# Kernel optimization log

Measured on AMD Instinct MI355X. Metric: run time of the kernel, lower is better.

## Reference

```python
import jax, jax.numpy as jnp
import numpy as np

HEADS = 16
HEAD_DIM = 128


def rotate_half(x):
    x1, x2 = x[..., : x.shape[-1] // 2], x[..., x.shape[-1] // 2 :]
    return jnp.concatenate((-x2, x1), axis=-1)


def setup_inputs() -> dict:
    key = jax.random.key(0)
    ks = jax.random.split(key, 8)
    b, s, h = 2, 2048, 2048
    d = HEAD_DIM
    sc = 1.0 / np.sqrt(h)
    x = jax.random.normal(ks[0], (b, s, h), jnp.float32)
    # real RoPE angles for realism
    inv_freq = 1.0 / (10000.0 ** (jnp.arange(0, d, 2, dtype=jnp.float32) / d))
    t = jnp.arange(s, dtype=jnp.float32)
    freqs = jnp.outer(t, inv_freq)  # [s, d/2]
    emb = jnp.concatenate((freqs, freqs), axis=-1)  # [s, d]
    return {
        "x": x,
        "cos": jnp.cos(emb),
        "sin": jnp.sin(emb),
        "wq": jax.random.normal(ks[1], (h, h), jnp.float32) * sc,
        "bq": jnp.zeros((h,), jnp.float32),
        "wk": jax.random.normal(ks[2], (h, h), jnp.float32) * sc,
        "bk": jnp.zeros((h,), jnp.float32),
        "wv": jax.random.normal(ks[3], (h, h), jnp.float32) * sc,
        "bv": jnp.zeros((h,), jnp.float32),
        "wo": jax.random.normal(ks[4], (h, h), jnp.float32) * sc,
    }


def reference(x, cos, sin, wq, bq, wk, bk, wv, bv, wo):
    b, s, hidden = x.shape
    nh, d = HEADS, HEAD_DIM
    # QKV projections (F.linear: x @ W.T + b)
    def split_heads(t):
        return t.reshape(b, s, nh, d).transpose(0, 2, 1, 3)  # [b,h,s,d]
    q = split_heads(x @ wq.T + bq)
    k = split_heads(x @ wk.T + bk)
    v = split_heads(x @ wv.T + bv)
    # RoPE (cos/sin: [s,d] broadcast over [b,h,s,d])
    q = q * cos + rotate_half(q) * sin
    k = k * cos + rotate_half(k) * sin
    # full (non-causal) attention, materializing [b,h,s,s] scores as original
    scale = 1.0 / jnp.sqrt(jnp.asarray(d, x.dtype))
    scores = jnp.einsum("bhqd,bhkd->bhqk", q, k) * scale
    attn = jax.nn.softmax(scores, axis=-1)
    out = jnp.einsum("bhqk,bhkd->bhqd", attn, v)  # [b,h,s,d]
    out = out.transpose(0, 2, 1, 3).reshape(b, s, hidden)
    # o_proj: no bias
    return out @ wo.T
```

## Files before the change

### kernel.cpp

```cpp
#include <hip/hip_runtime.h>

#define B_  2
#define NH  16
#define S_  2048
#define D_  128
#define HID 2048

typedef _Float16 half_t;
typedef _Float16 f16x8 __attribute__((ext_vector_type(8)));
typedef _Float16 f16x4_t __attribute__((ext_vector_type(4)));
typedef float f32x4 __attribute__((ext_vector_type(4)));

__device__ __forceinline__ void glds16(const half_t* g, half_t* l) {
    __builtin_amdgcn_global_load_lds(
        (const __attribute__((address_space(1))) void*)g,
        (__attribute__((address_space(3))) void*)l, 16, 0, 0);
}
__device__ __forceinline__ float fexp2(float x) { return __builtin_amdgcn_exp2f(x); }

__global__ __launch_bounds__(256) void cvt_all(
    const float* __restrict__ x,  const float* __restrict__ wq, const float* __restrict__ wk,
    const float* __restrict__ wv, const float* __restrict__ wo, half_t* __restrict__ dst)
{
    long i = ((long)blockIdx.x * 256 + threadIdx.x) * 4;
    const float* src; long off;
    if (i < 8388608)       { src = x;  off = i; }
    else if (i < 12582912) { src = wq; off = i - 8388608; }
    else if (i < 16777216) { src = wk; off = i - 12582912; }
    else if (i < 20971520) { src = wv; off = i - 16777216; }
    else                   { src = wo; off = i - 20971520; }
    float4 v = *(const float4*)(src + off);
    f16x4_t h;
    h[0] = (half_t)v.x; h[1] = (half_t)v.y; h[2] = (half_t)v.z; h[3] = (half_t)v.w;
    *(f16x4_t*)(dst + i) = h;
}

__global__ __launch_bounds__(256, 3) void qkv_gemm(
    const half_t* __restrict__ xb,
    const half_t* __restrict__ wqb, const half_t* __restrict__ wkb, const half_t* __restrict__ wvb,
    const float* __restrict__ bq, const float* __restrict__ bk, const float* __restrict__ bv,
    const float* __restrict__ cosp, const float* __restrict__ sinp,
    half_t* __restrict__ qo, half_t* __restrict__ ko, half_t* __restrict__ vto)
{
    __shared__ __align__(16) half_t As[128 * 32];
    __shared__ __align__(16) half_t Bs[128 * 32];
    const int m0 = blockIdx.x * 128;
    const int n0 = blockIdx.y * 128;
    const int z  = blockIdx.z;
    const half_t* wb   = (z == 0) ? wqb : (z == 1) ? wkb : wvb;
    const float*  bias = (z == 0) ? bq  : (z == 1) ? bk  : bv;
    const int tid = threadIdx.x, wave = tid >> 6, lane = tid & 63;
    const int quad = lane >> 4, lrow = lane & 15;
    const int wm = wave >> 1, wn = wave & 1;

    const int r0 = wave * 32 + (lane >> 2);
    const int r1 = r0 + 16;
    const int c0 = (((lane & 3) - (r0 >> 1)) & 3) * 8;
    const int c1 = (((lane & 3) - (r1 >> 1)) & 3) * 8;
    const half_t* ag0 = xb + (size_t)(m0 + r0) * HID + c0;
    const half_t* ag1 = xb + (size_t)(m0 + r1) * HID + c1;
    const half_t* bg0 = wb + (size_t)(n0 + r0) * HID + c0;
    const half_t* bg1 = wb + (size_t)(n0 + r1) * HID + c1;
    half_t* al0 = &As[(wave * 32) * 32];
    half_t* al1 = &As[(wave * 32 + 16) * 32];
    half_t* bl0 = &Bs[(wave * 32) * 32];
    half_t* bl1 = &Bs[(wave * 32 + 16) * 32];

    f32x4 acc[4][4] = {};

    for (int k0 = 0; k0 < HID; k0 += 32) {
        __syncthreads();
        glds16(ag0 + k0, al0);
        glds16(ag1 + k0, al1);
        glds16(bg0 + k0, bl0);
        glds16(bg1 + k0, bl1);
        __syncthreads();
        f16x8 af[4], bf[4];
#pragma unroll
        for (int mt = 0; mt < 4; mt++) {
            const int ra = wm * 64 + mt * 16 + lrow;
            const int pa = (quad + (ra >> 1)) & 3;
            af[mt] = *(const f16x8*)&As[ra * 32 + pa * 8];
        }
#pragma unroll
        for (int nt = 0; nt < 4; nt++) {
            const int rb = wn * 16 + nt * 32 + lrow;
            const int pb = (quad + (rb >> 1)) & 3;
            bf[nt] = *(const f16x8*)&Bs[rb * 32 + pb * 8];
        }
#pragma unroll
        for (int mt = 0; mt < 4; mt++)
#pragma unroll
            for (int nt = 0; nt < 4; nt++)
                acc[mt][nt] = __builtin_amdgcn_mfma_f32_16x16x32_f16(af[mt], bf[nt], acc[mt][nt], 0, 0, 0);
    }

    const int head = blockIdx.y;
    float bs_[4];
#pragma unroll
    for (int nt = 0; nt < 4; nt++) bs_[nt] = bias[n0 + nt * 32 + wn * 16 + lrow];
#pragma unroll
    for (int mt = 0; mt < 4; mt++) {
#pragma unroll
        for (int r = 0; r < 4; r++) {
            const int m  = m0 + wm * 64 + mt * 16 + quad * 4 + r;
            const int bb = m >> 11;
            const int st = m & (S_ - 1);
            float res[4];
#pragma unroll
            for (int nt = 0; nt < 4; nt++) res[nt] = acc[mt][nt][r] + bs_[nt];
            if (z < 2) {
                const float* cr = cosp + st * D_;
                const float* sr = sinp + st * D_;
#pragma unroll
                for (int pr = 0; pr < 2; pr++) {
                    const int dlo = pr * 32 + wn * 16 + lrow;
                    float cl = cr[dlo], sl = sr[dlo], ch = cr[dlo + 64], sh = sr[dlo + 64];
                    float lo = res[pr], hi = res[pr + 2];
                    res[pr]     = lo * cl - hi * sl;
                    res[pr + 2] = hi * ch + lo * sh;
                }
                half_t* dst = (z == 0 ? qo : ko) + ((size_t)(bb * NH + head) * S_ + st) * D_;
#pragma unroll
                for (int nt = 0; nt < 4; nt++) dst[nt * 32 + wn * 16 + lrow] = (half_t)res[nt];
            } else {
                half_t* dst = vto + (size_t)(bb * NH + head) * D_ * S_ + st;
#pragma unroll
                for (int nt = 0; nt < 4; nt++) dst[(size_t)(nt * 32 + wn * 16 + lrow) * S_] = (half_t)res[nt];
            }
        }
    }
}

#define PLD 72
__global__ __launch_bounds__(256, 2) void attn_kernel(
    const half_t* __restrict__ qb, const half_t* __restrict__ kb,
    const half_t* __restrict__ vtb, half_t* __restrict__ ob)
{
    __shared__ __align__(16) half_t ks[64 * 128];
    __shared__ __align__(16) half_t vs[128 * 64];
    __shared__ __align__(16) half_t ps[4 * 32 * PLD];
    const int head = blockIdx.y, b = blockIdx.z;
    const int bh = b * NH + head;
    const int tid = threadIdx.x, wave = tid >> 6, lane = tid & 63;
    const int quad = lane >> 4, lrow = lane & 15;
    const float SC = 0.08838834764831845f * 1.4426950408889634f;
    const int q0 = blockIdx.x * 128 + wave * 32;

    f16x8 qf[2][4];
#pragma unroll
    for (int mt = 0; mt < 2; mt++) {
        const half_t* qrow = qb + ((size_t)bh * S_ + q0 + mt * 16 + lrow) * D_;
#pragma unroll
        for (int kc = 0; kc < 4; kc++) {
            f16x8 v = *(const f16x8*)(qrow + kc * 32 + quad * 8);
#pragma unroll
            for (int j = 0; j < 8; j++) v[j] = (half_t)((float)v[j] * SC);
            qf[mt][kc] = v;
        }
    }

    const half_t* kbase = kb + (size_t)bh * S_ * D_;
    const half_t* vbase = vtb + (size_t)bh * D_ * S_;
    const int pbase = wave * 32 * PLD;

    float m_run[2] = {-1e30f, -1e30f}, l_run[2] = {0.f, 0.f};
    f32x4 o[2][8] = {};

    for (int kt = 0; kt < 32; kt++) {
        __syncthreads();
#pragma unroll
        for (int i = 0; i < 4; i++) {
            const int rk = wave * 16 + i * 4 + (lane >> 4);
            const int ck = (((lane & 15) - (rk & 7)) & 15) * 8;
            glds16(kbase + (size_t)(kt * 64 + rk) * D_ + ck, &ks[(wave * 16 + i * 4) * 128]);
            const int rv = wave * 32 + i * 8 + (lane >> 3);
            const int cv = (((lane & 7) - (rv & 7)) & 7) * 8;
            glds16(vbase + (size_t)rv * S_ + kt * 64 + cv, &vs[(wave * 32 + i * 8) * 64]);
        }
        __syncthreads();

        f32x4 st[2][4] = {};
#pragma unroll
        for (int nt = 0; nt < 4; nt++) {
            const int rk2 = nt * 16 + lrow;
#pragma unroll
            for (int kc = 0; kc < 4; kc++) {
                const int pk = (kc * 4 + quad + (rk2 & 7)) & 15;
                f16x8 kf = *(const f16x8*)&ks[rk2 * 128 + pk * 8];
                st[0][nt] = __builtin_amdgcn_mfma_f32_16x16x32_f16(kf, qf[0][kc], st[0][nt], 0, 0, 0);
                st[1][nt] = __builtin_amdgcn_mfma_f32_16x16x32_f16(kf, qf[1][kc], st[1][nt], 0, 0, 0);
            }
        }

        bool upd = false;
        float alpha[2];
#pragma unroll
        for (int mt = 0; mt < 2; mt++) {
            float m01 = fmaxf(fmaxf(st[mt][0][0], st[mt][0][1]), fmaxf(st[mt][0][2], st[mt][0][3]));
            float m11 = fmaxf(fmaxf(st[mt][1][0], st[mt][1][1]), fmaxf(st[mt][1][2], st[mt][1][3]));
            float m21 = fmaxf(fmaxf(st[mt][2][0], st[mt][2][1]), fmaxf(st[mt][2][2], st[mt][2][3]));
            float m31 = fmaxf(fmaxf(st[mt][3][0], st[mt][3][1]), fmaxf(st[mt][3][2], st[mt][3][3]));
            float mx = fmaxf(fmaxf(m01, m11), fmaxf(m21, m31));
            mx = fmaxf(mx, __shfl_xor(mx, 16));
            mx = fmaxf(mx, __shfl_xor(mx, 32));
            const float mnew = fmaxf(m_run[mt], mx);
            alpha[mt] = fexp2(m_run[mt] - mnew);
            upd = upd || (mnew > m_run[mt]);
            m_run[mt] = mnew;
            float rs = 0.f;
#pragma unroll
            for (int nt = 0; nt < 4; nt++) {
                f16x4_t pk4;
#pragma unroll
                for (int r = 0; r < 4; r++) {
                    float p = fexp2(st[mt][nt][r] - mnew);
                    rs += p;
                    pk4[r] = (half_t)p;
                }
                *(f16x4_t*)&ps[pbase + (mt * 16 + lrow) * PLD + nt * 16 + quad * 4] = pk4;
            }
            rs += __shfl_xor(rs, 16);
            rs += __shfl_xor(rs, 32);
            l_run[mt] = l_run[mt] * alpha[mt] + rs;
        }
        if (__any(upd)) {
#pragma unroll
            for (int mt = 0; mt < 2; mt++) {
                float ab[4];
#pragma unroll
                for (int r = 0; r < 4; r++) ab[r] = __shfl(alpha[mt], quad * 4 + r, 16);
#pragma unroll
                for (int dt = 0; dt < 8; dt++)
#pragma unroll
                    for (int r = 0; r < 4; r++) o[mt][dt][r] *= ab[r];
            }
        }

#pragma unroll
        for (int kc2 = 0; kc2 < 2; kc2++) {
            f16x8 pf0 = *(const f16x8*)&ps[pbase + lrow * PLD + kc2 * 32 + quad * 8];
            f16x8 pf1 = *(const f16x8*)&ps[pbase + (16 + lrow) * PLD + kc2 * 32 + quad * 8];
#pragma unroll
            for (int dt = 0; dt < 8; dt++) {
                const int rv2 = dt * 16 + lrow;
                const int pv = (kc2 * 4 + quad + (rv2 & 7)) & 7;
                f16x8 vf = *(const f16x8*)&vs[rv2 * 64 + pv * 8];
                o[0][dt] = __builtin_amdgcn_mfma_f32_16x16x32_f16(pf0, vf, o[0][dt], 0, 0, 0);
                o[1][dt] = __builtin_amdgcn_mfma_f32_16x16x32_f16(pf1, vf, o[1][dt], 0, 0, 0);
            }
        }
    }

#pragma unroll
    for (int mt = 0; mt < 2; mt++) {
        const float rl = 1.f / l_run[mt];
        float rb[4];
#pragma unroll
        for (int r = 0; r < 4; r++) rb[r] = __shfl(rl, quad * 4 + r, 16);
#pragma unroll
        for (int dt = 0; dt < 8; dt++) {
            const int d = dt * 16 + lrow;
#pragma unroll
            for (int r = 0; r < 4; r++) {
                const int row = q0 + mt * 16 + quad * 4 + r;
                ob[((size_t)b * S_ + row) * HID + head * D_ + d] = (half_t)(o[mt][dt][r] * rb[r]);
            }
        }
    }
}

__global__ __launch_bounds__(256, 3) void out_gemm(
    const half_t* __restrict__ ab, const half_t* __restrict__ wob, float* __restrict__ out)
{
    __shared__ __align__(16) half_t As[128 * 32];
    __shared__ __align__(16) half_t Bs[128 * 32];
    const int m0 = blockIdx.x * 128;
    const int n0 = blockIdx.y * 128;
    const int tid = threadIdx.x, wave = tid >> 6, lane = tid & 63;
    const int quad = lane >> 4, lrow = lane & 15;
    const int wm = wave >> 1, wn = wave & 1;

    const int r0 = wave * 32 + (lane >> 2);
    const int r1 = r0 + 16;
    const int c0 = (((lane & 3) - (r0 >> 1)) & 3) * 8;
    const int c1 = (((lane & 3) - (r1 >> 1)) & 3) * 8;
    const half_t* ag0 = ab  + (size_t)(m0 + r0) * HID + c0;
    const half_t* ag1 = ab  + (size_t)(m0 + r1) * HID + c1;
    const half_t* bg0 = wob + (size_t)(n0 + r0) * HID + c0;
    const half_t* bg1 = wob + (size_t)(n0 + r1) * HID + c1;
    half_t* al0 = &As[(wave * 32) * 32];
    half_t* al1 = &As[(wave * 32 + 16) * 32];
    half_t* bl0 = &Bs[(wave * 32) * 32];
    half_t* bl1 = &Bs[(wave * 32 + 16) * 32];

    f32x4 acc[4][4] = {};

    for (int k0 = 0; k0 < HID; k0 += 32) {
        __syncthreads();
        glds16(ag0 + k0, al0);
        glds16(ag1 + k0, al1);
        glds16(bg0 + k0, bl0);
        glds16(bg1 + k0, bl1);
        __syncthreads();
        f16x8 af[4], bf[4];
#pragma unroll
        for (int mt = 0; mt < 4; mt++) {
            const int ra = wm * 64 + mt * 16 + lrow;
            const int pa = (quad + (ra >> 1)) & 3;
            af[mt] = *(const f16x8*)&As[ra * 32 + pa * 8];
        }
#pragma unroll
        for (int nt = 0; nt < 4; nt++) {
            const int rb = wn * 16 + nt * 32 + lrow;
            const int pb = (quad + (rb >> 1)) & 3;
            bf[nt] = *(const f16x8*)&Bs[rb * 32 + pb * 8];
        }
#pragma unroll
        for (int mt = 0; mt < 4; mt++)
#pragma unroll
            for (int nt = 0; nt < 4; nt++)
                acc[mt][nt] = __builtin_amdgcn_mfma_f32_16x16x32_f16(af[mt], bf[nt], acc[mt][nt], 0, 0, 0);
    }

#pragma unroll
    for (int mt = 0; mt < 4; mt++)
#pragma unroll
        for (int r = 0; r < 4; r++) {
            const int m = m0 + wm * 64 + mt * 16 + quad * 4 + r;
#pragma unroll
            for (int nt = 0; nt < 4; nt++)
                out[(size_t)m * HID + n0 + nt * 32 + wn * 16 + lrow] = acc[mt][nt][r];
        }
}

extern "C" void kernel_launch(void* const* d_in, const int* in_sizes, int n_in,
                              void* d_out, int out_size, void* d_ws, size_t ws_size,
                              hipStream_t stream)
{
    const float* x    = (const float*)d_in[0];
    const float* cosp = (const float*)d_in[1];
    const float* sinp = (const float*)d_in[2];
    const float* wq   = (const float*)d_in[3];
    const float* bq   = (const float*)d_in[4];
    const float* wk   = (const float*)d_in[5];
    const float* bk   = (const float*)d_in[6];
    const float* wv   = (const float*)d_in[7];
    const float* bv   = (const float*)d_in[8];
    const float* wo   = (const float*)d_in[9];
    float* out = (float*)d_out;

    half_t* w   = (half_t*)d_ws;
    half_t* xb  = w;
    half_t* wqb = xb  + 8388608;
    half_t* wkb = wqb + 4194304;
    half_t* wvb = wkb + 4194304;
    half_t* wob = wvb + 4194304;
    half_t* qo  = wob + 4194304;
    half_t* ko  = qo  + 8388608;
    half_t* vto = ko  + 8388608;
    half_t* ob  = vto + 8388608;

    cvt_all<<<24576, 256, 0, stream>>>(x, wq, wk, wv, wo, xb);
    qkv_gemm<<<dim3(32, 16, 3), 256, 0, stream>>>(xb, wqb, wkb, wvb, bq, bk, bv,
                                                  cosp, sinp, qo, ko, vto);
    attn_kernel<<<dim3(16, 16, 2), 256, 0, stream>>>(qo, ko, vto, ob);
    out_gemm<<<dim3(32, 16), 256, 0, stream>>>(ob, wob, out);
}
```

Before: 434.3 us.

## Rewrite QKV GEMM with 256x128 tiles and triple-buffered async LDS pipeline

```diff
diff --git a/kernel.cpp b/kernel.cpp
--- a/kernel.cpp
+++ b/kernel.cpp
@@ -35,98 +35,142 @@
     *(f16x4_t*)(dst + i) = h;
 }
 
-__global__ __launch_bounds__(256, 3) void qkv_gemm(
+__global__ __launch_bounds__(512, 2) void qkv_gemm(
     const half_t* __restrict__ xb,
     const half_t* __restrict__ wqb, const half_t* __restrict__ wkb, const half_t* __restrict__ wvb,
     const float* __restrict__ bq, const float* __restrict__ bk, const float* __restrict__ bv,
     const float* __restrict__ cosp, const float* __restrict__ sinp,
     half_t* __restrict__ qo, half_t* __restrict__ ko, half_t* __restrict__ vto)
 {
-    __shared__ __align__(16) half_t As[128 * 32];
-    __shared__ __align__(16) half_t Bs[128 * 32];
-    const int m0 = blockIdx.x * 128;
+    __shared__ __align__(16) half_t As[3][256 * 64];
+    __shared__ __align__(16) half_t Bs[3][128 * 64];
+    const int m0 = blockIdx.x * 256;
     const int n0 = blockIdx.y * 128;
     const int z  = blockIdx.z;
     const half_t* wb   = (z == 0) ? wqb : (z == 1) ? wkb : wvb;
     const float*  bias = (z == 0) ? bq  : (z == 1) ? bk  : bv;
-    const int tid = threadIdx.x, wave = tid >> 6, lane = tid & 63;
-    const int quad = lane >> 4, lrow = lane & 15;
-    const int wm = wave >> 1, wn = wave & 1;
-
-    const int r0 = wave * 32 + (lane >> 2);
-    const int r1 = r0 + 16;
-    const int c0 = (((lane & 3) - (r0 >> 1)) & 3) * 8;
-    const int c1 = (((lane & 3) - (r1 >> 1)) & 3) * 8;
-    const half_t* ag0 = xb + (size_t)(m0 + r0) * HID + c0;
-    const half_t* ag1 = xb + (size_t)(m0 + r1) * HID + c1;
-    const half_t* bg0 = wb + (size_t)(n0 + r0) * HID + c0;
-    const half_t* bg1 = wb + (size_t)(n0 + r1) * HID + c1;
-    half_t* al0 = &As[(wave * 32) * 32];
-    half_t* al1 = &As[(wave * 32 + 16) * 32];
-    half_t* bl0 = &Bs[(wave * 32) * 32];
-    half_t* bl1 = &Bs[(wave * 32 + 16) * 32];
-
-    f32x4 acc[4][4] = {};
-
-    for (int k0 = 0; k0 < HID; k0 += 32) {
-        __syncthreads();
-        glds16(ag0 + k0, al0);
-        glds16(ag1 + k0, al1);
-        glds16(bg0 + k0, bl0);
-        glds16(bg1 + k0, bl1);
-        __syncthreads();
-        f16x8 af[4], bf[4];
-#pragma unroll
-        for (int mt = 0; mt < 4; mt++) {
-            const int ra = wm * 64 + mt * 16 + lrow;
-            const int pa = (quad + (ra >> 1)) & 3;
-            af[mt] = *(const f16x8*)&As[ra * 32 + pa * 8];
-        }
-#pragma unroll
-        for (int nt = 0; nt < 4; nt++) {
-            const int rb = wn * 16 + nt * 32 + lrow;
-            const int pb = (quad + (rb >> 1)) & 3;
-            bf[nt] = *(const f16x8*)&Bs[rb * 32 + pb * 8];
-        }
-#pragma unroll
-        for (int mt = 0; mt < 4; mt++)
-#pragma unroll
-            for (int nt = 0; nt < 4; nt++)
-                acc[mt][nt] = __builtin_amdgcn_mfma_f32_16x16x32_f16(af[mt], bf[nt], acc[mt][nt], 0, 0, 0);
+
+    const int tid = threadIdx.x, w = tid >> 6, l = tid & 63;
+    const int lrow = l & 15, quad = l >> 4;
+    const int wm = w >> 2, wn = w & 3;
+    const int srow = w * 8 + (l >> 3);
+    const int c8   = ((l & 7) - (l >> 3)) & 7;
+    const half_t* asrc = xb + (size_t)(m0 + srow) * HID + c8 * 8;
+    const half_t* bsrc = wb + (size_t)(n0 + srow) * HID + c8 * 8;
+
+    const int pc0 = (quad + (lrow & 7)) & 7;
+    const int pc1 = (4 + quad + (lrow & 7)) & 7;
+
+    f32x4 acc[8][2] = {};
+
+    auto STA = [&](int buf, int t) {
+        const half_t* s = asrc + t * 64;
+        half_t* d = &As[buf][(w * 8) * 64];
+#pragma unroll
+        for (int j = 0; j < 4; ++j)
+            glds16(s + (size_t)j * 64 * HID, d + j * 64 * 64);
+    };
+    auto STB = [&](int buf, int t) {
+        const half_t* s = bsrc + t * 64;
+        half_t* d = &Bs[buf][(w * 8) * 64];
+#pragma unroll
+        for (int j = 0; j < 2; ++j)
+            glds16(s + (size_t)j * 64 * HID, d + j * 64 * 64);
+    };
+
+    STA(0, 0); STB(0, 0);
+    STA(1, 1); STB(1, 1);
+    asm volatile("s_waitcnt vmcnt(6)" ::: "memory");
+    __syncthreads();
+
+    f16x8 af[8], bf[4];
+    int buf = 0;
+    for (int t = 0; t < 32; ++t) {
+        const int sb = (buf >= 1) ? buf - 1 : 2;
+        const half_t* Ab = As[buf];
+        const half_t* Bb = Bs[buf];
+
+        if (t + 2 < 32) STA(sb, t + 2);
+#pragma unroll
+        for (int mt2 = 0; mt2 < 4; ++mt2) {
+            const int ra = wm * 128 + mt2 * 16 + lrow;
+            af[mt2 * 2 + 0] = *(const f16x8*)&Ab[ra * 64 + pc0 * 8];
+            af[mt2 * 2 + 1] = *(const f16x8*)&Ab[ra * 64 + pc1 * 8];
+        }
+#pragma unroll
+        for (int ntl = 0; ntl < 2; ++ntl) {
+            const int rb = ntl * 64 + wn * 16 + lrow;
+            bf[ntl * 2 + 0] = *(const f16x8*)&Bb[rb * 64 + pc0 * 8];
+            bf[ntl * 2 + 1] = *(const f16x8*)&Bb[rb * 64 + pc1 * 8];
+        }
+        __builtin_amdgcn_s_barrier();
+        asm volatile("s_waitcnt lgkmcnt(0)" ::: "memory");
+        __builtin_amdgcn_sched_barrier(0);
+        __builtin_amdgcn_s_setprio(1);
+#pragma unroll
+        for (int mt2 = 0; mt2 < 4; ++mt2)
+#pragma unroll
+            for (int ntl = 0; ntl < 2; ++ntl) {
+                acc[mt2][ntl] = __builtin_amdgcn_mfma_f32_16x16x32_f16(af[mt2*2],   bf[ntl*2],   acc[mt2][ntl], 0, 0, 0);
+                acc[mt2][ntl] = __builtin_amdgcn_mfma_f32_16x16x32_f16(af[mt2*2+1], bf[ntl*2+1], acc[mt2][ntl], 0, 0, 0);
+            }
+        __builtin_amdgcn_s_setprio(0);
+        __builtin_amdgcn_sched_barrier(0);
+        __builtin_amdgcn_s_barrier();
+
+        if (t + 2 < 32) STB(sb, t + 2);
+#pragma unroll
+        for (int mt2 = 0; mt2 < 4; ++mt2) {
+            const int ra = wm * 128 + 64 + mt2 * 16 + lrow;
+            af[mt2 * 2 + 0] = *(const f16x8*)&Ab[ra * 64 + pc0 * 8];
+            af[mt2 * 2 + 1] = *(const f16x8*)&Ab[ra * 64 + pc1 * 8];
+        }
+        if (t < 30) asm volatile("s_waitcnt vmcnt(6)" ::: "memory");
+        else        asm volatile("s_waitcnt vmcnt(0)" ::: "memory");
+        __builtin_amdgcn_s_barrier();
+        asm volatile("s_waitcnt lgkmcnt(0)" ::: "memory");
+        __builtin_amdgcn_sched_barrier(0);
+        __builtin_amdgcn_s_setprio(1);
+#pragma unroll
+        for (int mt2 = 0; mt2 < 4; ++mt2)
+#pragma unroll
+            for (int ntl = 0; ntl < 2; ++ntl) {
+                acc[4+mt2][ntl] = __builtin_amdgcn_mfma_f32_16x16x32_f16(af[mt2*2],   bf[ntl*2],   acc[4+mt2][ntl], 0, 0, 0);
+                acc[4+mt2][ntl] = __builtin_amdgcn_mfma_f32_16x16x32_f16(af[mt2*2+1], bf[ntl*2+1], acc[4+mt2][ntl], 0, 0, 0);
+            }
+        __builtin_amdgcn_s_setprio(0);
+        __builtin_amdgcn_sched_barrier(0);
+        __builtin_amdgcn_s_barrier();
+
+        buf = (buf == 2) ? 0 : buf + 1;
     }
 
     const int head = blockIdx.y;
-    float bs_[4];
-#pragma unroll
-    for (int nt = 0; nt < 4; nt++) bs_[nt] = bias[n0 + nt * 32 + wn * 16 + lrow];
-#pragma unroll
-    for (int mt = 0; mt < 4; mt++) {
-#pragma unroll
-        for (int r = 0; r < 4; r++) {
-            const int m  = m0 + wm * 64 + mt * 16 + quad * 4 + r;
+    const int colL = wn * 16 + lrow;
+    const float bsL = bias[n0 + colL];
+    const float bsH = bias[n0 + 64 + colL];
+#pragma unroll
+    for (int mt = 0; mt < 8; ++mt) {
+#pragma unroll
+        for (int r = 0; r < 4; ++r) {
+            const int m  = m0 + wm * 128 + mt * 16 + quad * 4 + r;
             const int bb = m >> 11;
             const int st = m & (S_ - 1);
-            float res[4];
-#pragma unroll
-            for (int nt = 0; nt < 4; nt++) res[nt] = acc[mt][nt][r] + bs_[nt];
+            float lo = acc[mt][0][r] + bsL;
+            float hi = acc[mt][1][r] + bsH;
             if (z < 2) {
                 const float* cr = cosp + st * D_;
                 const float* sr = sinp + st * D_;
-#pragma unroll
-                for (int pr = 0; pr < 2; pr++) {
-                    const int dlo = pr * 32 + wn * 16 + lrow;
-                    float cl = cr[dlo], sl = sr[dlo], ch = cr[dlo + 64], sh = sr[dlo + 64];
-                    float lo = res[pr], hi = res[pr + 2];
-                    res[pr]     = lo * cl - hi * sl;
-                    res[pr + 2] = hi * ch + lo * sh;
-                }
+                float cl = cr[colL], sl = sr[colL], ch = cr[colL + 64], sh = sr[colL + 64];
+                float olo = lo * cl - hi * sl;
+                float ohi = hi * ch + lo * sh;
                 half_t* dst = (z == 0 ? qo : ko) + ((size_t)(bb * NH + head) * S_ + st) * D_;
-#pragma unroll
-                for (int nt = 0; nt < 4; nt++) dst[nt * 32 + wn * 16 + lrow] = (half_t)res[nt];
+                dst[colL]      = (half_t)olo;
+                dst[colL + 64] = (half_t)ohi;
             } else {
                 half_t* dst = vto + (size_t)(bb * NH + head) * D_ * S_ + st;
-#pragma unroll
-                for (int nt = 0; nt < 4; nt++) dst[(size_t)(nt * 32 + wn * 16 + lrow) * S_] = (half_t)res[nt];
+                dst[(size_t)colL * S_]        = (half_t)lo;
+                dst[(size_t)(colL + 64) * S_] = (half_t)hi;
             }
         }
     }
@@ -362,7 +406,7 @@
     half_t* ob  = vto + 8388608;
 
     cvt_all<<<24576, 256, 0, stream>>>(x, wq, wk, wv, wo, xb);
-    qkv_gemm<<<dim3(32, 16, 3), 256, 0, stream>>>(xb, wqb, wkb, wvb, bq, bk, bv,
+    qkv_gemm<<<dim3(16, 16, 3), 512, 0, stream>>>(xb, wqb, wkb, wvb, bq, bk, bv,
                                                   cosp, sinp, qo, ko, vto);
     attn_kernel<<<dim3(16, 16, 2), 256, 0, stream>>>(qo, ko, vto, ob);
     out_gemm<<<dim3(32, 16), 256, 0, stream>>>(ob, wob, out);
```

Measured after the change: 456.9 us. +5.2%, slower.
